# Kernel optimization log

Hardware: AMD Instinct MI355X
Metric: run time of the kernel (lower is better)

Reference implementation:

```python
import jax, jax.numpy as jnp
import numpy as np

B, S, D, H = 2, 2048, 2048, 16
HD = D // H


def setup_inputs() -> dict:
    key = jax.random.key(0)
    ks = jax.random.split(key, 9)
    s = 1.0 / np.sqrt(D)
    return {
        "hidden_states": jax.random.normal(ks[0], (B, S, D), dtype=jnp.float32),
        "attention_mask": jnp.ones((B, 1, 1, S), dtype=jnp.int32),
        "Wq": jax.random.normal(ks[1], (D, D), dtype=jnp.float32) * s,
        "bq": jnp.zeros((D,), dtype=jnp.float32),
        "Wk": jax.random.normal(ks[2], (D, D), dtype=jnp.float32) * s,
        "bk": jnp.zeros((D,), dtype=jnp.float32),
        "Wv": jax.random.normal(ks[3], (D, D), dtype=jnp.float32) * s,
        "bv": jnp.zeros((D,), dtype=jnp.float32),
        "Wo": jax.random.normal(ks[4], (D, D), dtype=jnp.float32) * s,
        "bo": jnp.zeros((D,), dtype=jnp.float32),
    }


def reference(hidden_states, attention_mask, Wq, bq, Wk, bk, Wv, bv, Wo, bo):
    scale = 1.0 / np.sqrt(HD)
    # projections: torch Linear is x @ W.T + b
    q = hidden_states @ Wq.T + bq
    k = hidden_states @ Wk.T + bk
    v = hidden_states @ Wv.T + bv
    # [B,S,D] -> [B,H,S,hd]
    q = q.reshape(B, S, H, HD).transpose(0, 2, 1, 3)
    k = k.reshape(B, S, H, HD).transpose(0, 2, 1, 3)
    v = v.reshape(B, S, H, HD).transpose(0, 2, 1, 3)
    scores = jnp.einsum("bhqd,bhkd->bhqk", q, k) * scale
    scores = jnp.where(attention_mask == 0, jnp.float32(-1e9), scores)
    probs = jax.nn.softmax(scores, axis=-1)
    attn = jnp.einsum("bhqk,bhkd->bhqd", probs, v)
    attn = attn.transpose(0, 2, 1, 3).reshape(B, S, D)
    out = attn @ Wo.T + bo
    return out
```

## Files before the change

kernel.cpp:

```cpp
#include <hip/hip_runtime.h>
#include <hip/hip_bf16.h>
#include <stdint.h>

typedef __attribute__((ext_vector_type(8))) short short8;
typedef __attribute__((ext_vector_type(8))) unsigned short ushort8;
typedef __attribute__((ext_vector_type(4))) float f32x4;

#define DEVI __device__ __forceinline__

DEVI unsigned short f2bf(float f) {
    union { float f; unsigned int u; } a;
    a.f = f;
    unsigned int u = a.u;
    u += 0x7fffu + ((u >> 16) & 1u);
    return (unsigned short)(u >> 16);
}

DEVI void stage16(const unsigned short* g, unsigned short* ldsbase) {
    __builtin_amdgcn_global_load_lds(
        (const __attribute__((address_space(1))) void*)(uintptr_t)g,
        (__attribute__((address_space(3))) void*)(uintptr_t)ldsbase,
        16, 0, 0);
}

__global__ void cast_all(const float* __restrict__ hs, const float* __restrict__ wq,
                         const float* __restrict__ wk, const float* __restrict__ wv,
                         const float* __restrict__ wo, unsigned short* __restrict__ dst) {
    int i = blockIdx.x * blockDim.x + threadIdx.x;
    const float* src;
    int local;
    if (i < 1048576) { src = hs; local = i; }
    else {
        int j = i - 1048576;
        int w = j >> 19;
        local = j & 524287;
        src = (w == 0) ? wq : (w == 1) ? wk : (w == 2) ? wv : wo;
    }
    const float4* s = (const float4*)src;
    float4 x = s[2 * local], y = s[2 * local + 1];
    ushort8 o;
    o[0] = f2bf(x.x); o[1] = f2bf(x.y); o[2] = f2bf(x.z); o[3] = f2bf(x.w);
    o[4] = f2bf(y.x); o[5] = f2bf(y.y); o[6] = f2bf(y.z); o[7] = f2bf(y.w);
    *(ushort8*)(dst + 8 * i) = o;
}

#define QSCALE 0.12751879523173862f

__launch_bounds__(256, 3)
__global__ void gemm_qkv(const unsigned short* __restrict__ A, const unsigned short* __restrict__ Bstack,
                         const float* __restrict__ bq, const float* __restrict__ bk,
                         const float* __restrict__ bv, unsigned short* __restrict__ qb,
                         unsigned short* __restrict__ kb, unsigned short* __restrict__ vtb) {
    constexpr int K = 2048;
    __shared__ __align__(16) unsigned short As[2 * 4096];
    __shared__ __align__(16) unsigned short Bs[2 * 4096];
    const int tid = threadIdx.x;
    const int lane = tid & 63, wid = tid >> 6;
    const int quad = lane >> 4, l15 = lane & 15;
    const int m0 = blockIdx.y * 128, n0 = blockIdx.x * 128;
    const int mode = n0 >> 11;
    const int wm = (wid & 1) * 64, wn = (wid >> 1) * 64;

    f32x4 acc[4][4];
#pragma unroll
    for (int i = 0; i < 4; i++)
#pragma unroll
        for (int j = 0; j < 4; j++) acc[i][j] = f32x4{0.f, 0.f, 0.f, 0.f};

    const int s0 = wid * 128 + lane, s1 = s0 + 64;
    const int r0 = s0 >> 2, c0 = (s0 & 3) ^ (r0 & 3);
    const int r1 = s1 >> 2, c1 = (s1 & 3) ^ (r1 & 3);
    const int ldsoffA0 = wid * 1024, ldsoffA1 = wid * 1024 + 512;
    const unsigned short* Ag0 = &A[(m0 + r0) * K + c0 * 8];
    const unsigned short* Ag1 = &A[(m0 + r1) * K + c1 * 8];
    const unsigned short* Bg0 = &Bstack[(n0 + r0) * K + c0 * 8];
    const unsigned short* Bg1 = &Bstack[(n0 + r1) * K + c1 * 8];

    stage16(Ag0, &As[ldsoffA0]);
    stage16(Ag1, &As[ldsoffA1]);
    stage16(Bg0, &Bs[ldsoffA0]);
    stage16(Bg1, &Bs[ldsoffA1]);

    for (int i = 0; i < 64; i++) {
        const int cur = (i & 1) * 4096;
        asm volatile("s_waitcnt vmcnt(0)" ::: "memory");
        __syncthreads();
        if (i < 63) {
            const int nxt = 4096 - cur;
            const int koff = (i + 1) * 32;
            stage16(Ag0 + koff, &As[nxt + ldsoffA0]);
            stage16(Ag1 + koff, &As[nxt + ldsoffA1]);
            stage16(Bg0 + koff, &Bs[nxt + ldsoffA0]);
            stage16(Bg1 + koff, &Bs[nxt + ldsoffA1]);
        }
        short8 af[4], bfr[4];
#pragma unroll
        for (int mi = 0; mi < 4; mi++) {
            int row = wm + mi * 16 + l15;
            int cc = quad ^ (row & 3);
            af[mi] = *(const short8*)&As[cur + row * 32 + cc * 8];
        }
#pragma unroll
        for (int ni = 0; ni < 4; ni++) {
            int row = wn + ni * 16 + l15;
            int cc = quad ^ (row & 3);
            bfr[ni] = *(const short8*)&Bs[cur + row * 32 + cc * 8];
        }
#pragma unroll
        for (int mi = 0; mi < 4; mi++)
#pragma unroll
            for (int ni = 0; ni < 4; ni++)
                acc[mi][ni] = __builtin_amdgcn_mfma_f32_16x16x32_bf16(af[mi], bfr[ni], acc[mi][ni], 0, 0, 0);
    }

    const float* bias = (mode == 0) ? bq : (mode == 1) ? bk : bv;
#pragma unroll
    for (int mi = 0; mi < 4; mi++) {
#pragma unroll
        for (int ni = 0; ni < 4; ni++) {
            int n = n0 + wn + ni * 16 + l15;
            int nl = n & 2047;
            float bb = bias[nl];
            if (mode == 2) {
                int m_base = m0 + wm + mi * 16 + quad * 4;
                int h = nl >> 7, dd = nl & 127, bbb = m_base >> 11, s = m_base & 2047;
                unsigned int v0 = f2bf(acc[mi][ni][0] + bb) | ((unsigned int)f2bf(acc[mi][ni][1] + bb) << 16);
                unsigned int v1 = f2bf(acc[mi][ni][2] + bb) | ((unsigned int)f2bf(acc[mi][ni][3] + bb) << 16);
                uint2 pk; pk.x = v0; pk.y = v1;
                *(uint2*)&vtb[((bbb * 16 + h) * 128 + dd) * 2048 + s] = pk;
            } else {
                unsigned short* dst = (mode == 0) ? qb : kb;
                float sc = (mode == 0) ? QSCALE : 1.0f;
#pragma unroll
                for (int r = 0; r < 4; r++) {
                    int m = m0 + wm + mi * 16 + quad * 4 + r;
                    dst[m * 2048 + nl] = f2bf((acc[mi][ni][r] + bb) * sc);
                }
            }
        }
    }
}

__launch_bounds__(256, 2)
__global__ void gemm_out(const unsigned short* __restrict__ A, const unsigned short* __restrict__ Bw,
                         const float* __restrict__ bias, float* __restrict__ Cout) {
    constexpr int K = 2048;
    __shared__ __align__(16) unsigned short As[2 * 4096];
    __shared__ __align__(16) unsigned short Bs[2 * 4096];
    const int tid = threadIdx.x;
    const int lane = tid & 63, wid = tid >> 6;
    const int quad = lane >> 4, l15 = lane & 15;
    const int m0 = blockIdx.y * 128, n0 = blockIdx.x * 128;
    const int wm = (wid & 1) * 64, wn = (wid >> 1) * 64;

    f32x4 acc[4][4];
#pragma unroll
    for (int i = 0; i < 4; i++)
#pragma unroll
        for (int j = 0; j < 4; j++) acc[i][j] = f32x4{0.f, 0.f, 0.f, 0.f};

    const int s0 = wid * 128 + lane, s1 = s0 + 64;
    const int r0 = s0 >> 2, c0 = (s0 & 3) ^ (r0 & 3);
    const int r1 = s1 >> 2, c1 = (s1 & 3) ^ (r1 & 3);
    const int ldsoffA0 = wid * 1024, ldsoffA1 = wid * 1024 + 512;
    const unsigned short* Ag0 = &A[(m0 + r0) * K + c0 * 8];
    const unsigned short* Ag1 = &A[(m0 + r1) * K + c1 * 8];
    const unsigned short* Bg0 = &Bw[(n0 + r0) * K + c0 * 8];
    const unsigned short* Bg1 = &Bw[(n0 + r1) * K + c1 * 8];

    stage16(Ag0, &As[ldsoffA0]);
    stage16(Ag1, &As[ldsoffA1]);
    stage16(Bg0, &Bs[ldsoffA0]);
    stage16(Bg1, &Bs[ldsoffA1]);

    for (int i = 0; i < 64; i++) {
        const int cur = (i & 1) * 4096;
        asm volatile("s_waitcnt vmcnt(0)" ::: "memory");
        __syncthreads();
        if (i < 63) {
            const int nxt = 4096 - cur;
            const int koff = (i + 1) * 32;
            stage16(Ag0 + koff, &As[nxt + ldsoffA0]);
            stage16(Ag1 + koff, &As[nxt + ldsoffA1]);
            stage16(Bg0 + koff, &Bs[nxt + ldsoffA0]);
            stage16(Bg1 + koff, &Bs[nxt + ldsoffA1]);
        }
        short8 af[4], bfr[4];
#pragma unroll
        for (int mi = 0; mi < 4; mi++) {
            int row = wm + mi * 16 + l15;
            int cc = quad ^ (row & 3);
            af[mi] = *(const short8*)&As[cur + row * 32 + cc * 8];
        }
#pragma unroll
        for (int ni = 0; ni < 4; ni++) {
            int row = wn + ni * 16 + l15;
            int cc = quad ^ (row & 3);
            bfr[ni] = *(const short8*)&Bs[cur + row * 32 + cc * 8];
        }
#pragma unroll
        for (int mi = 0; mi < 4; mi++)
#pragma unroll
            for (int ni = 0; ni < 4; ni++)
                acc[mi][ni] = __builtin_amdgcn_mfma_f32_16x16x32_bf16(af[mi], bfr[ni], acc[mi][ni], 0, 0, 0);
    }

#pragma unroll
    for (int mi = 0; mi < 4; mi++) {
#pragma unroll
        for (int ni = 0; ni < 4; ni++) {
            int n = n0 + wn + ni * 16 + l15;
            float bb = bias[n];
#pragma unroll
            for (int r = 0; r < 4; r++) {
                int m = m0 + wm + mi * 16 + quad * 4 + r;
                Cout[m * 2048 + n] = acc[mi][ni][r] + bb;
            }
        }
    }
}

__launch_bounds__(512, 1)
__global__ void attn_fused(const unsigned short* __restrict__ Q, const unsigned short* __restrict__ Kb,
                           const unsigned short* __restrict__ VT, const int* __restrict__ mask,
                           unsigned short* __restrict__ Ob) {
    __shared__ __align__(16) unsigned short Ks[2][64 * 128];
    __shared__ __align__(16) unsigned short Vs[2][128 * 64];
    __shared__ __align__(16) unsigned short Ps[8][32 * 72];
    __shared__ int Ms[2048];

    const int tid = threadIdx.x;
    const int lane = tid & 63, wid = tid >> 6;
    const int quad = lane >> 4, l15 = lane & 15;
    const int qt = blockIdx.x, bh = blockIdx.y;
    const int b = bh >> 4, h = bh & 15;
    const int tok0 = b * 2048 + qt * 256 + wid * 32;

    for (int i = tid; i < 2048; i += 512) Ms[i] = mask[b * 2048 + i];

    short8 aq[2][4];
#pragma unroll
    for (int mi = 0; mi < 2; mi++)
#pragma unroll
        for (int c = 0; c < 4; c++)
            aq[mi][c] = *(const short8*)&Q[(tok0 + mi * 16 + l15) * 2048 + h * 128 + c * 32 + quad * 8];

    f32x4 oacc[2][8];
#pragma unroll
    for (int mi = 0; mi < 2; mi++)
#pragma unroll
        for (int c = 0; c < 8; c++) oacc[mi][c] = f32x4{0.f, 0.f, 0.f, 0.f};
    float lacc[2][4] = {{0.f, 0.f, 0.f, 0.f}, {0.f, 0.f, 0.f, 0.f}};

    const unsigned short* Kbase = Kb + b * 2048 * 2048 + h * 128;
    const unsigned short* Vbase = VT + (b * 16 + h) * 128 * 2048;

    const unsigned short* KgP[2];
    const unsigned short* VgP[2];
    int ldsKoff[2], ldsVoff[2];
#pragma unroll
    for (int j = 0; j < 2; j++) {
        int s = wid * 128 + j * 64 + lane;
        int kr = s >> 4, kc = (s & 15) ^ (kr & 7);
        int vr = s >> 3, vc = (s & 7) ^ (vr & 7);
        KgP[j] = Kbase + kr * 2048 + kc * 8;
        VgP[j] = Vbase + vr * 2048 + vc * 8;
        ldsKoff[j] = (wid * 128 + j * 64) * 8;
        ldsVoff[j] = (wid * 128 + j * 64) * 8;
    }
    unsigned short* pw = &Ps[wid][0];

#pragma unroll
    for (int j = 0; j < 2; j++) {
        stage16(KgP[j], &Ks[0][ldsKoff[j]]);
        stage16(VgP[j], &Vs[0][ldsVoff[j]]);
    }

    for (int kt = 0; kt < 32; kt++) {
        const int cur = kt & 1;
        const int key0 = kt * 64;
        asm volatile("s_waitcnt vmcnt(0)" ::: "memory");
        __syncthreads();
        if (kt < 31) {
            const int nb = cur ^ 1;
            const int key0n = key0 + 64;
#pragma unroll
            for (int j = 0; j < 2; j++) {
                stage16(KgP[j] + key0n * 2048, &Ks[nb][ldsKoff[j]]);
                stage16(VgP[j] + key0n, &Vs[nb][ldsVoff[j]]);
            }
        }
        int mk[4];
#pragma unroll
        for (int t = 0; t < 4; t++) mk[t] = Ms[key0 + t * 16 + l15];

        f32x4 sc[2][4];
#pragma unroll
        for (int mi = 0; mi < 2; mi++)
#pragma unroll
            for (int t = 0; t < 4; t++) sc[mi][t] = f32x4{0.f, 0.f, 0.f, 0.f};
#pragma unroll
        for (int c = 0; c < 4; c++)
#pragma unroll
            for (int t = 0; t < 4; t++) {
                int row = t * 16 + l15;
                int cc = (4 * c + quad) ^ (row & 7);
                short8 bk = *(const short8*)&Ks[cur][row * 128 + cc * 8];
                sc[0][t] = __builtin_amdgcn_mfma_f32_16x16x32_bf16(aq[0][c], bk, sc[0][t], 0, 0, 0);
                sc[1][t] = __builtin_amdgcn_mfma_f32_16x16x32_bf16(aq[1][c], bk, sc[1][t], 0, 0, 0);
            }

#pragma unroll
        for (int mi = 0; mi < 2; mi++)
#pragma unroll
            for (int t = 0; t < 4; t++)
#pragma unroll
                for (int r = 0; r < 4; r++) {
                    float cs = mk[t] ? sc[mi][t][r] : -1e30f;
                    float p = __builtin_amdgcn_exp2f(cs);
                    lacc[mi][r] += p;
                    pw[(mi * 16 + quad * 4 + r) * 72 + t * 16 + l15] = f2bf(p);
                }
        asm volatile("s_waitcnt lgkmcnt(0)" ::: "memory");
        short8 ap[2][2];
#pragma unroll
        for (int mi = 0; mi < 2; mi++)
#pragma unroll
            for (int kk = 0; kk < 2; kk++)
                ap[mi][kk] = *(const short8*)&pw[(mi * 16 + l15) * 72 + kk * 32 + quad * 8];

#pragma unroll
        for (int kk = 0; kk < 2; kk++)
#pragma unroll
            for (int dt = 0; dt < 8; dt++) {
                int row = dt * 16 + l15;
                int cc = (kk * 4 + quad) ^ (row & 7);
                short8 bv = *(const short8*)&Vs[cur][row * 64 + cc * 8];
                oacc[0][dt] = __builtin_amdgcn_mfma_f32_16x16x32_bf16(ap[0][kk], bv, oacc[0][dt], 0, 0, 0);
                oacc[1][dt] = __builtin_amdgcn_mfma_f32_16x16x32_bf16(ap[1][kk], bv, oacc[1][dt], 0, 0, 0);
            }
    }

    float inv[2][4];
#pragma unroll
    for (int mi = 0; mi < 2; mi++)
#pragma unroll
        for (int r = 0; r < 4; r++) {
            float l = lacc[mi][r];
#pragma unroll
            for (int off = 1; off < 16; off <<= 1) l += __shfl_xor(l, off, 64);
            inv[mi][r] = 1.0f / l;
        }
#pragma unroll
    for (int mi = 0; mi < 2; mi++)
#pragma unroll
        for (int dt = 0; dt < 8; dt++)
#pragma unroll
            for (int r = 0; r < 4; r++) {
                float val = oacc[mi][dt][r] * inv[mi][r];
                Ob[(tok0 + mi * 16 + quad * 4 + r) * 2048 + h * 128 + dt * 16 + l15] = f2bf(val);
            }
}

extern "C" void kernel_launch(void* const* d_in, const int* in_sizes, int n_in,
                              void* d_out, int out_size, void* d_ws, size_t ws_size,
                              hipStream_t stream) {
    const float* hs = (const float*)d_in[0];
    const int* mask = (const int*)d_in[1];
    const float* Wq = (const float*)d_in[2];
    const float* bq = (const float*)d_in[3];
    const float* Wk = (const float*)d_in[4];
    const float* bk = (const float*)d_in[5];
    const float* Wv = (const float*)d_in[6];
    const float* bv = (const float*)d_in[7];
    const float* Wo = (const float*)d_in[8];
    const float* bo = (const float*)d_in[9];

    unsigned short* hsb = (unsigned short*)d_ws;
    unsigned short* wqb = hsb + 8388608;
    unsigned short* wob = wqb + 3 * 4194304;
    unsigned short* qb  = wob + 4194304;
    unsigned short* kb  = qb  + 8388608;
    unsigned short* vtb = kb  + 8388608;
    unsigned short* ab  = vtb + 8388608;

    cast_all<<<12288, 256, 0, stream>>>(hs, Wq, Wk, Wv, Wo, hsb);

    gemm_qkv<<<dim3(48, 32), 256, 0, stream>>>(hsb, wqb, bq, bk, bv, qb, kb, vtb);
    attn_fused<<<dim3(8, 32), 512, 0, stream>>>(qb, kb, vtb, mask, ab);
    gemm_out<<<dim3(16, 32), 256, 0, stream>>>(ab, wob, bo, (float*)d_out);
}
```

Baseline: 400.6 us.

## Restructure QKV GEMM into 256x256 tiles with 8-wave interleaved load/MFMA pipeline

The QKV projection GEMM moves from 128x128 tiles with 4 waves and K-step 32 to 256x256 tiles with 8 waves and K-step 64. Each K iteration is split into four quadrant phases, and global-to-LDS loads for half-tiles are staged in between MFMA bursts. The phases are separated by barriers, s_setprio and sched_barrier. This is meant to raise arithmetic intensity and overlap memory traffic with compute. The cost is much more LDS (128KB per block), more accumulator registers, and only 384 blocks for the device's compute units.

```diff
diff --git a/kernel.cpp b/kernel.cpp
--- a/kernel.cpp
+++ b/kernel.cpp
@@ -46,76 +46,165 @@
 
 #define QSCALE 0.12751879523173862f
 
-__launch_bounds__(256, 3)
+DEVI void stageg(const unsigned short* gT, unsigned short* ldsTile, int wrow0, int kcol) {
+    stage16(gT + wrow0 * 2048 + kcol, ldsTile + wrow0 * 64);
+}
+
+__launch_bounds__(512, 2)
 __global__ void gemm_qkv(const unsigned short* __restrict__ A, const unsigned short* __restrict__ Bstack,
                          const float* __restrict__ bq, const float* __restrict__ bk,
                          const float* __restrict__ bv, unsigned short* __restrict__ qb,
                          unsigned short* __restrict__ kb, unsigned short* __restrict__ vtb) {
-    constexpr int K = 2048;
-    __shared__ __align__(16) unsigned short As[2 * 4096];
-    __shared__ __align__(16) unsigned short Bs[2 * 4096];
+    constexpr int K = 2048, NT = 32;
+    __shared__ __align__(16) unsigned short As[2][16384];
+    __shared__ __align__(16) unsigned short Bs[2][16384];
     const int tid = threadIdx.x;
     const int lane = tid & 63, wid = tid >> 6;
     const int quad = lane >> 4, l15 = lane & 15;
-    const int m0 = blockIdx.y * 128, n0 = blockIdx.x * 128;
+    const int m0 = blockIdx.y * 256, n0 = blockIdx.x * 256;
     const int mode = n0 >> 11;
-    const int wm = (wid & 1) * 64, wn = (wid >> 1) * 64;
-
-    f32x4 acc[4][4];
-#pragma unroll
-    for (int i = 0; i < 4; i++)
+    const int wm = (wid & 1) * 128, wn = (wid >> 1) * 64;
+
+    const int wa = wid * 8;
+    const int wb = (wid >> 2) * 64 + (wid & 3) * 8;
+    const int rib = lane >> 3;
+    const int cg = (lane & 7) ^ rib;
+    const unsigned short* AgT = A + (m0 + rib) * K + cg * 8;
+    const unsigned short* BgT = Bstack + (n0 + rib) * K + cg * 8;
+
+    f32x4 acc[8][4];
+#pragma unroll
+    for (int i = 0; i < 8; i++)
 #pragma unroll
         for (int j = 0; j < 4; j++) acc[i][j] = f32x4{0.f, 0.f, 0.f, 0.f};
 
-    const int s0 = wid * 128 + lane, s1 = s0 + 64;
-    const int r0 = s0 >> 2, c0 = (s0 & 3) ^ (r0 & 3);
-    const int r1 = s1 >> 2, c1 = (s1 & 3) ^ (r1 & 3);
-    const int ldsoffA0 = wid * 1024, ldsoffA1 = wid * 1024 + 512;
-    const unsigned short* Ag0 = &A[(m0 + r0) * K + c0 * 8];
-    const unsigned short* Ag1 = &A[(m0 + r1) * K + c1 * 8];
-    const unsigned short* Bg0 = &Bstack[(n0 + r0) * K + c0 * 8];
-    const unsigned short* Bg1 = &Bstack[(n0 + r1) * K + c1 * 8];
-
-    stage16(Ag0, &As[ldsoffA0]);
-    stage16(Ag1, &As[ldsoffA1]);
-    stage16(Bg0, &Bs[ldsoffA0]);
-    stage16(Bg1, &Bs[ldsoffA1]);
-
-    for (int i = 0; i < 64; i++) {
-        const int cur = (i & 1) * 4096;
-        asm volatile("s_waitcnt vmcnt(0)" ::: "memory");
-        __syncthreads();
-        if (i < 63) {
-            const int nxt = 4096 - cur;
-            const int koff = (i + 1) * 32;
-            stage16(Ag0 + koff, &As[nxt + ldsoffA0]);
-            stage16(Ag1 + koff, &As[nxt + ldsoffA1]);
-            stage16(Bg0 + koff, &Bs[nxt + ldsoffA0]);
-            stage16(Bg1 + koff, &Bs[nxt + ldsoffA1]);
-        }
-        short8 af[4], bfr[4];
+    stageg(AgT, As[0], wa, 0);       stageg(AgT, As[0], 128 + wa, 0);
+    stageg(BgT, Bs[0], wb, 0);       stageg(BgT, Bs[0], 128 + wb, 0);
+    stageg(BgT, Bs[0], 32 + wb, 0);  stageg(BgT, Bs[0], 160 + wb, 0);
+    stageg(AgT, As[0], 64 + wa, 0);  stageg(AgT, As[0], 192 + wa, 0);
+    stageg(AgT, As[1], wa, 64);      stageg(AgT, As[1], 128 + wa, 64);
+    stageg(BgT, Bs[1], wb, 64);      stageg(BgT, Bs[1], 128 + wb, 64);
+    asm volatile("s_waitcnt vmcnt(4)" ::: "memory");
+    __builtin_amdgcn_s_barrier();
+
+    short8 af[4][2], bf0[2][2], bf1[2][2];
+    for (int i = 0; i < NT; i++) {
+        const int cur = i & 1, nxt = cur ^ 1;
+        const unsigned short* Ac = As[cur];
+        const unsigned short* Bc = Bs[cur];
+
 #pragma unroll
         for (int mi = 0; mi < 4; mi++) {
             int row = wm + mi * 16 + l15;
-            int cc = quad ^ (row & 3);
-            af[mi] = *(const short8*)&As[cur + row * 32 + cc * 8];
-        }
-#pragma unroll
-        for (int ni = 0; ni < 4; ni++) {
+#pragma unroll
+            for (int kw = 0; kw < 2; kw++) {
+                int cc = (kw * 4 + quad) ^ (row & 7);
+                af[mi][kw] = *(const short8*)&Ac[row * 64 + cc * 8];
+            }
+        }
+#pragma unroll
+        for (int ni = 0; ni < 2; ni++) {
             int row = wn + ni * 16 + l15;
-            int cc = quad ^ (row & 3);
-            bfr[ni] = *(const short8*)&Bs[cur + row * 32 + cc * 8];
-        }
-#pragma unroll
-        for (int mi = 0; mi < 4; mi++)
-#pragma unroll
-            for (int ni = 0; ni < 4; ni++)
-                acc[mi][ni] = __builtin_amdgcn_mfma_f32_16x16x32_bf16(af[mi], bfr[ni], acc[mi][ni], 0, 0, 0);
+#pragma unroll
+            for (int kw = 0; kw < 2; kw++) {
+                int cc = (kw * 4 + quad) ^ (row & 7);
+                bf0[ni][kw] = *(const short8*)&Bc[row * 64 + cc * 8];
+            }
+        }
+        if (i + 1 < NT) {
+            stageg(BgT, Bs[nxt], 32 + wb, (i + 1) * 64);
+            stageg(BgT, Bs[nxt], 160 + wb, (i + 1) * 64);
+        }
+        __builtin_amdgcn_s_barrier();
+        asm volatile("s_waitcnt lgkmcnt(0)" ::: "memory");
+        __builtin_amdgcn_sched_barrier(0);
+        __builtin_amdgcn_s_setprio(1);
+#pragma unroll
+        for (int kw = 0; kw < 2; kw++)
+#pragma unroll
+            for (int mi = 0; mi < 4; mi++)
+#pragma unroll
+                for (int ni = 0; ni < 2; ni++)
+                    acc[mi][ni] = __builtin_amdgcn_mfma_f32_16x16x32_bf16(af[mi][kw], bf0[ni][kw], acc[mi][ni], 0, 0, 0);
+        __builtin_amdgcn_s_setprio(0);
+        __builtin_amdgcn_s_barrier();
+
+#pragma unroll
+        for (int ni = 0; ni < 2; ni++) {
+            int row = wn + 32 + ni * 16 + l15;
+#pragma unroll
+            for (int kw = 0; kw < 2; kw++) {
+                int cc = (kw * 4 + quad) ^ (row & 7);
+                bf1[ni][kw] = *(const short8*)&Bc[row * 64 + cc * 8];
+            }
+        }
+        if (i + 1 < NT) {
+            stageg(AgT, As[nxt], 64 + wa, (i + 1) * 64);
+            stageg(AgT, As[nxt], 192 + wa, (i + 1) * 64);
+        }
+        __builtin_amdgcn_s_barrier();
+        asm volatile("s_waitcnt lgkmcnt(0)" ::: "memory");
+        __builtin_amdgcn_sched_barrier(0);
+        __builtin_amdgcn_s_setprio(1);
+#pragma unroll
+        for (int kw = 0; kw < 2; kw++)
+#pragma unroll
+            for (int mi = 0; mi < 4; mi++)
+#pragma unroll
+                for (int ni = 0; ni < 2; ni++)
+                    acc[mi][2 + ni] = __builtin_amdgcn_mfma_f32_16x16x32_bf16(af[mi][kw], bf1[ni][kw], acc[mi][2 + ni], 0, 0, 0);
+        __builtin_amdgcn_s_setprio(0);
+        __builtin_amdgcn_s_barrier();
+
+#pragma unroll
+        for (int mi = 0; mi < 4; mi++) {
+            int row = wm + 64 + mi * 16 + l15;
+#pragma unroll
+            for (int kw = 0; kw < 2; kw++) {
+                int cc = (kw * 4 + quad) ^ (row & 7);
+                af[mi][kw] = *(const short8*)&Ac[row * 64 + cc * 8];
+            }
+        }
+        if (i + 2 < NT) {
+            stageg(AgT, As[cur], wa, (i + 2) * 64);
+            stageg(AgT, As[cur], 128 + wa, (i + 2) * 64);
+        }
+        __builtin_amdgcn_s_barrier();
+        asm volatile("s_waitcnt lgkmcnt(0)" ::: "memory");
+        __builtin_amdgcn_sched_barrier(0);
+        __builtin_amdgcn_s_setprio(1);
+#pragma unroll
+        for (int kw = 0; kw < 2; kw++)
+#pragma unroll
+            for (int mi = 0; mi < 4; mi++)
+#pragma unroll
+                for (int ni = 0; ni < 2; ni++)
+                    acc[4 + mi][2 + ni] = __builtin_amdgcn_mfma_f32_16x16x32_bf16(af[mi][kw], bf1[ni][kw], acc[4 + mi][2 + ni], 0, 0, 0);
+        __builtin_amdgcn_s_setprio(0);
+        __builtin_amdgcn_s_barrier();
+
+        if (i + 2 < NT) {
+            stageg(BgT, Bs[cur], wb, (i + 2) * 64);
+            stageg(BgT, Bs[cur], 128 + wb, (i + 2) * 64);
+        }
+        if (i < NT - 2) asm volatile("s_waitcnt vmcnt(4)" ::: "memory");
+        else            asm volatile("s_waitcnt vmcnt(0)" ::: "memory");
+        __builtin_amdgcn_s_barrier();
+        __builtin_amdgcn_s_setprio(1);
+#pragma unroll
+        for (int kw = 0; kw < 2; kw++)
+#pragma unroll
+            for (int mi = 0; mi < 4; mi++)
+#pragma unroll
+                for (int ni = 0; ni < 2; ni++)
+                    acc[4 + mi][ni] = __builtin_amdgcn_mfma_f32_16x16x32_bf16(af[mi][kw], bf0[ni][kw], acc[4 + mi][ni], 0, 0, 0);
+        __builtin_amdgcn_s_setprio(0);
+        __builtin_amdgcn_s_barrier();
     }
 
     const float* bias = (mode == 0) ? bq : (mode == 1) ? bk : bv;
 #pragma unroll
-    for (int mi = 0; mi < 4; mi++) {
+    for (int mi = 0; mi < 8; mi++) {
 #pragma unroll
         for (int ni = 0; ni < 4; ni++) {
             int n = n0 + wn + ni * 16 + l15;
@@ -386,7 +475,7 @@
 
     cast_all<<<12288, 256, 0, stream>>>(hs, Wq, Wk, Wv, Wo, hsb);
 
-    gemm_qkv<<<dim3(48, 32), 256, 0, stream>>>(hsb, wqb, bq, bk, bv, qb, kb, vtb);
+    gemm_qkv<<<dim3(24, 16), 512, 0, stream>>>(hsb, wqb, bq, bk, bv, qb, kb, vtb);
     attn_fused<<<dim3(8, 32), 512, 0, stream>>>(qb, kb, vtb, mask, ab);
     gemm_out<<<dim3(16, 32), 256, 0, stream>>>(ab, wob, bo, (float*)d_out);
 }
```

Result: faster. 380.8 us (-4.9%).

## Enlarge QKV GEMM tiles to 256x384 with 8 waves and deeper prefetch

Applied to the files above, without the earlier changes.

Restructures the fused QKV projection GEMM to use 512-thread blocks computing 256x384 output tiles, with each wave holding an 8x6 grid of MFMA accumulators. This raises data reuse per LDS load and cuts the grid to one block per CU. Global-to-LDS staging now prefetches two k-steps ahead, with a partial vmcnt wait, and s_setprio is raised around the MFMA bursts. The XOR LDS swizzle is dropped, which may add bank conflicts. The larger accumulator set adds register pressure, and because tiles straddle the Q/K/V boundaries, the output mode is now chosen per column.

```diff
diff --git a/kernel.cpp b/kernel.cpp
--- a/kernel.cpp
+++ b/kernel.cpp
@@ -46,82 +46,96 @@
 
 #define QSCALE 0.12751879523173862f
 
-__launch_bounds__(256, 3)
+__launch_bounds__(512, 2)
 __global__ void gemm_qkv(const unsigned short* __restrict__ A, const unsigned short* __restrict__ Bstack,
                          const float* __restrict__ bq, const float* __restrict__ bk,
                          const float* __restrict__ bv, unsigned short* __restrict__ qb,
                          unsigned short* __restrict__ kb, unsigned short* __restrict__ vtb) {
-    constexpr int K = 2048;
-    __shared__ __align__(16) unsigned short As[2 * 4096];
-    __shared__ __align__(16) unsigned short Bs[2 * 4096];
+    constexpr int K = 2048, NT = 64;
+    __shared__ __align__(16) unsigned short AB[2][20480];
     const int tid = threadIdx.x;
     const int lane = tid & 63, wid = tid >> 6;
     const int quad = lane >> 4, l15 = lane & 15;
-    const int m0 = blockIdx.y * 128, n0 = blockIdx.x * 128;
-    const int mode = n0 >> 11;
-    const int wm = (wid & 1) * 64, wn = (wid >> 1) * 64;
-
-    f32x4 acc[4][4];
-#pragma unroll
-    for (int i = 0; i < 4; i++)
-#pragma unroll
-        for (int j = 0; j < 4; j++) acc[i][j] = f32x4{0.f, 0.f, 0.f, 0.f};
-
-    const int s0 = wid * 128 + lane, s1 = s0 + 64;
-    const int r0 = s0 >> 2, c0 = (s0 & 3) ^ (r0 & 3);
-    const int r1 = s1 >> 2, c1 = (s1 & 3) ^ (r1 & 3);
-    const int ldsoffA0 = wid * 1024, ldsoffA1 = wid * 1024 + 512;
-    const unsigned short* Ag0 = &A[(m0 + r0) * K + c0 * 8];
-    const unsigned short* Ag1 = &A[(m0 + r1) * K + c1 * 8];
-    const unsigned short* Bg0 = &Bstack[(n0 + r0) * K + c0 * 8];
-    const unsigned short* Bg1 = &Bstack[(n0 + r1) * K + c1 * 8];
-
-    stage16(Ag0, &As[ldsoffA0]);
-    stage16(Ag1, &As[ldsoffA1]);
-    stage16(Bg0, &Bs[ldsoffA0]);
-    stage16(Bg1, &Bs[ldsoffA1]);
-
-    for (int i = 0; i < 64; i++) {
-        const int cur = (i & 1) * 4096;
-        asm volatile("s_waitcnt vmcnt(0)" ::: "memory");
-        __syncthreads();
-        if (i < 63) {
-            const int nxt = 4096 - cur;
-            const int koff = (i + 1) * 32;
-            stage16(Ag0 + koff, &As[nxt + ldsoffA0]);
-            stage16(Ag1 + koff, &As[nxt + ldsoffA1]);
-            stage16(Bg0 + koff, &Bs[nxt + ldsoffA0]);
-            stage16(Bg1 + koff, &Bs[nxt + ldsoffA1]);
-        }
-        short8 af[4], bfr[4];
-#pragma unroll
-        for (int mi = 0; mi < 4; mi++) {
-            int row = wm + mi * 16 + l15;
-            int cc = quad ^ (row & 3);
-            af[mi] = *(const short8*)&As[cur + row * 32 + cc * 8];
-        }
-#pragma unroll
-        for (int ni = 0; ni < 4; ni++) {
-            int row = wn + ni * 16 + l15;
-            int cc = quad ^ (row & 3);
-            bfr[ni] = *(const short8*)&Bs[cur + row * 32 + cc * 8];
-        }
+    const int m0 = blockIdx.y * 256, n0 = blockIdx.x * 384;
+    const int wm = (wid >> 2) * 128, wn = (wid & 3) * 96;
+
+    const int rr = lane >> 2, kc = lane & 3;
+    const unsigned short* AgT = A + (m0 + rr) * K + kc * 8;
+    const unsigned short* BgT = Bstack + (n0 + rr) * K + kc * 8;
+
+    f32x4 acc[8][6];
+#pragma unroll
+    for (int i = 0; i < 8; i++)
+#pragma unroll
+        for (int j = 0; j < 6; j++) acc[i][j] = f32x4{0.f, 0.f, 0.f, 0.f};
+
+#pragma unroll
+    for (int t = 0; t < 2; t++) {
+        unsigned short* cb = &AB[t][0];
+        const int koff = t * 32;
+        stage16(AgT + (wid) * 16 * K + koff,      cb + (wid) * 512);
+        stage16(AgT + (wid + 8) * 16 * K + koff,  cb + (wid + 8) * 512);
+        stage16(BgT + (wid) * 16 * K + koff,      cb + 8192 + (wid) * 512);
+        stage16(BgT + (wid + 8) * 16 * K + koff,  cb + 8192 + (wid + 8) * 512);
+        stage16(BgT + (wid + 16) * 16 * K + koff, cb + 8192 + (wid + 16) * 512);
+    }
+
+    short8 af[4], bf[6];
+    for (int i = 0; i < NT; i++) {
+        const int cur = i & 1;
+        unsigned short* cb = &AB[cur][0];
+
+        if (i < NT - 1) asm volatile("s_waitcnt vmcnt(5)" ::: "memory");
+        else            asm volatile("s_waitcnt vmcnt(0)" ::: "memory");
+        __builtin_amdgcn_s_barrier();
+
 #pragma unroll
         for (int mi = 0; mi < 4; mi++)
-#pragma unroll
-            for (int ni = 0; ni < 4; ni++)
-                acc[mi][ni] = __builtin_amdgcn_mfma_f32_16x16x32_bf16(af[mi], bfr[ni], acc[mi][ni], 0, 0, 0);
-    }
-
-    const float* bias = (mode == 0) ? bq : (mode == 1) ? bk : bv;
-#pragma unroll
-    for (int mi = 0; mi < 4; mi++) {
-#pragma unroll
-        for (int ni = 0; ni < 4; ni++) {
+            af[mi] = *(const short8*)&cb[(wm + mi * 16 + l15) * 32 + quad * 8];
+#pragma unroll
+        for (int ni = 0; ni < 6; ni++)
+            bf[ni] = *(const short8*)&cb[8192 + (wn + ni * 16 + l15) * 32 + quad * 8];
+        __builtin_amdgcn_s_setprio(1);
+#pragma unroll
+        for (int mi = 0; mi < 4; mi++)
+#pragma unroll
+            for (int ni = 0; ni < 6; ni++)
+                acc[mi][ni] = __builtin_amdgcn_mfma_f32_16x16x32_bf16(af[mi], bf[ni], acc[mi][ni], 0, 0, 0);
+        __builtin_amdgcn_s_setprio(0);
+
+#pragma unroll
+        for (int mi = 0; mi < 4; mi++)
+            af[mi] = *(const short8*)&cb[(wm + 64 + mi * 16 + l15) * 32 + quad * 8];
+        __builtin_amdgcn_s_setprio(1);
+#pragma unroll
+        for (int mi = 0; mi < 4; mi++)
+#pragma unroll
+            for (int ni = 0; ni < 6; ni++)
+                acc[4 + mi][ni] = __builtin_amdgcn_mfma_f32_16x16x32_bf16(af[mi], bf[ni], acc[4 + mi][ni], 0, 0, 0);
+        __builtin_amdgcn_s_setprio(0);
+
+        __builtin_amdgcn_s_barrier();
+        asm volatile("" ::: "memory");
+
+        if (i + 2 < NT) {
+            const int koff = (i + 2) * 32;
+            stage16(AgT + (wid) * 16 * K + koff,      cb + (wid) * 512);
+            stage16(AgT + (wid + 8) * 16 * K + koff,  cb + (wid + 8) * 512);
+            stage16(BgT + (wid) * 16 * K + koff,      cb + 8192 + (wid) * 512);
+            stage16(BgT + (wid + 8) * 16 * K + koff,  cb + 8192 + (wid + 8) * 512);
+            stage16(BgT + (wid + 16) * 16 * K + koff, cb + 8192 + (wid + 16) * 512);
+        }
+    }
+
+#pragma unroll
+    for (int mi = 0; mi < 8; mi++) {
+#pragma unroll
+        for (int ni = 0; ni < 6; ni++) {
             int n = n0 + wn + ni * 16 + l15;
+            int md = n >> 11;
             int nl = n & 2047;
-            float bb = bias[nl];
-            if (mode == 2) {
+            float bb = ((md == 0) ? bq : (md == 1) ? bk : bv)[nl];
+            if (md == 2) {
                 int m_base = m0 + wm + mi * 16 + quad * 4;
                 int h = nl >> 7, dd = nl & 127, bbb = m_base >> 11, s = m_base & 2047;
                 unsigned int v0 = f2bf(acc[mi][ni][0] + bb) | ((unsigned int)f2bf(acc[mi][ni][1] + bb) << 16);
@@ -129,8 +143,8 @@
                 uint2 pk; pk.x = v0; pk.y = v1;
                 *(uint2*)&vtb[((bbb * 16 + h) * 128 + dd) * 2048 + s] = pk;
             } else {
-                unsigned short* dst = (mode == 0) ? qb : kb;
-                float sc = (mode == 0) ? QSCALE : 1.0f;
+                unsigned short* dst = (md == 0) ? qb : kb;
+                float sc = (md == 0) ? QSCALE : 1.0f;
 #pragma unroll
                 for (int r = 0; r < 4; r++) {
                     int m = m0 + wm + mi * 16 + quad * 4 + r;
@@ -386,7 +400,7 @@
 
     cast_all<<<12288, 256, 0, stream>>>(hs, Wq, Wk, Wv, Wo, hsb);
 
-    gemm_qkv<<<dim3(48, 32), 256, 0, stream>>>(hsb, wqb, bq, bk, bv, qb, kb, vtb);
+    gemm_qkv<<<dim3(16, 16), 512, 0, stream>>>(hsb, wqb, bq, bk, bv, qb, kb, vtb);
     attn_fused<<<dim3(8, 32), 512, 0, stream>>>(qb, kb, vtb, mask, ab);
     gemm_out<<<dim3(16, 32), 256, 0, stream>>>(ab, wob, bo, (float*)d_out);
 }
```

Measured after the change: 383.6 us. -4.2%, faster.
